# Kernel tuning notes

Measured on AMD Instinct MI355X. Metric: run time of the kernel, lower is better.

Reference implementation:

```python
import jax, jax.numpy as jnp
import numpy as np

ITERATIONS = 3
EPS = 1e-06

def squash(s):
    # square_norm along last dim, keepdims (matches torch squash)
    sq = jnp.sum(s * s, axis=-1, keepdims=True)
    return sq / (1.0 + sq) * s / (jnp.sqrt(sq) + EPS)

def setup_inputs() -> dict:
    key = jax.random.key(0)
    k1, k2 = jax.random.split(key)
    x = jax.random.normal(k1, (64, 32, 8, 8, 16), dtype=jnp.float32)
    W = jax.random.normal(k2, (1, 32, 8, 8, 32, 16, 32), dtype=jnp.float32)
    return {"x": x, "W": W}

def reference(x, W):
    # u_hat: (B, C, H, Wd, O, D) = x (B,C,H,Wd,I) @ W (C,H,Wd,O,I,D)
    u_hat = jnp.einsum('bchwi,chwoid->bchwod', x, W[0])
    b = jnp.zeros(u_hat.shape[:-1], dtype=u_hat.dtype)  # (B,C,H,Wd,O)
    for _ in range(ITERATIONS - 1):
        c = jax.nn.softmax(b, axis=-1)
        s = jnp.sum(c[..., None] * u_hat, axis=(1, 2, 3))  # (B,O,D)
        v = squash(s)
        b = b + jnp.sum(u_hat * v[:, None, None, None], axis=-1)
    c = jax.nn.softmax(b, axis=-1)
    s = jnp.sum(c[..., None] * u_hat, axis=(1, 2, 3))
    return squash(s)  # (B, out_capsules, out_cap_dim)
```

## Files before the change

### kernel.cpp

```cpp
#include <hip/hip_runtime.h>
#include <math.h>

#define B_ 64
#define N_ 2048
#define O_ 32
#define I_ 16
#define D_ 32
#define OD_ 1024

typedef __attribute__((ext_vector_type(8))) short bf16x8;
typedef __attribute__((ext_vector_type(4))) float f32x4;

union FragU { unsigned u[4]; uint4 v; bf16x8 f; };

__device__ __forceinline__ void barrier_lds() {
  asm volatile("s_waitcnt lgkmcnt(0)\n\ts_barrier" ::: "memory");
}

template <int CTRL>
__device__ __forceinline__ float dpp_mov_f(float x) {
  return __int_as_float(
      __builtin_amdgcn_update_dpp(0, __float_as_int(x), CTRL, 0xf, 0xf, true));
}
__device__ __forceinline__ float row16_sum(float x) {
  x += dpp_mov_f<0x128>(x);
  x += dpp_mov_f<0x124>(x);
  x += dpp_mov_f<0x4e>(x);
  x += dpp_mov_f<0xb1>(x);
  return x;
}
__device__ __forceinline__ float grp32_max(float x) {
  x = fmaxf(x, dpp_mov_f<0xb1>(x));
  x = fmaxf(x, dpp_mov_f<0x4e>(x));
  x = fmaxf(x, dpp_mov_f<0x124>(x));
  x = fmaxf(x, dpp_mov_f<0x128>(x));
  x = fmaxf(x, __shfl_xor(x, 16));
  return x;
}
__device__ __forceinline__ float grp32_sum(float x) {
  x += dpp_mov_f<0xb1>(x);
  x += dpp_mov_f<0x4e>(x);
  x += dpp_mov_f<0x124>(x);
  x += dpp_mov_f<0x128>(x);
  x += __shfl_xor(x, 16);
  return x;
}

__device__ __forceinline__ void dk_split(float f, unsigned &h, unsigned &l) {
  unsigned u = __float_as_uint(f);
  h = u & 0xffff0000u;
  float lo = f - __uint_as_float(h);
  l = __float_as_uint(lo) >> 16;
}
__device__ __forceinline__ void dk_split16(float f, unsigned short &h,
                                           unsigned short &l) {
  unsigned u = __float_as_uint(f);
  unsigned hu = u & 0xffff0000u;
  h = (unsigned short)(u >> 16);
  float lo = f - __uint_as_float(hu);
  l = (unsigned short)(__float_as_uint(lo) >> 16);
}
__device__ __forceinline__ unsigned pk(unsigned short e0, unsigned short e1) {
  return (unsigned)e0 | ((unsigned)e1 << 16);
}

__global__ __launch_bounds__(256) void prep_all(const float* __restrict__ W,
                                                const float* __restrict__ x,
                                                uint4* __restrict__ WP,
                                                uint4* __restrict__ XP) {
  if (blockIdx.x < 8192) {
    int t = blockIdx.x * 256 + threadIdx.x;
    int d = t & 31, o = (t >> 5) & 31, n = t >> 10;
    const float* wp = W + ((size_t)(n * O_ + o) * I_) * D_ + d;
    unsigned short hh[I_], ll[I_];
#pragma unroll
    for (int i = 0; i < I_; ++i) dk_split16(wp[i * D_], hh[i], ll[i]);
    int c = d & 15, dhalf = d >> 4;
    size_t base = ((size_t)(n * O_ + o) * 2 + dhalf) * 4;
#pragma unroll
    for (int sel = 0; sel < 2; ++sel) {
      const unsigned short* e = sel ? ll : hh;
#pragma unroll
      for (int qp = 0; qp < 2; ++qp) {
        uint4 u;
        u.x = pk(e[qp * 8 + 0], e[qp * 8 + 1]);
        u.y = pk(e[qp * 8 + 2], e[qp * 8 + 3]);
        u.z = pk(e[qp * 8 + 4], e[qp * 8 + 5]);
        u.w = pk(e[qp * 8 + 6], e[qp * 8 + 7]);
        WP[(base + sel * 2 + qp) * 16 + c] = u;
      }
    }
  } else {
    int t = (blockIdx.x - 8192) * 256 + threadIdx.x;
    int c = t & 15, n = (t >> 4) & 2047, bg = t >> 15;
    const float* xp = x + ((size_t)(bg * 16 + c) * N_ + n) * I_;
    unsigned short hh[I_], ll[I_];
#pragma unroll
    for (int i = 0; i < I_; ++i) dk_split16(xp[i], hh[i], ll[i]);
    size_t base = ((size_t)bg * N_ + n) * 4;
#pragma unroll
    for (int sel = 0; sel < 2; ++sel) {
      const unsigned short* e = sel ? ll : hh;
#pragma unroll
      for (int qp = 0; qp < 2; ++qp) {
        uint4 u;
        u.x = pk(e[qp * 8 + 0], e[qp * 8 + 1]);
        u.y = pk(e[qp * 8 + 2], e[qp * 8 + 3]);
        u.z = pk(e[qp * 8 + 4], e[qp * 8 + 5]);
        u.w = pk(e[qp * 8 + 6], e[qp * 8 + 7]);
        XP[(base + sel * 2 + qp) * 16 + c] = u;
      }
    }
  }
}

template <int UNIFORM>
__global__ __launch_bounds__(1024, 4) void mfma_pass6(
    const uint4* __restrict__ XP, const uint4* __restrict__ WP,
    const float* __restrict__ v, float* __restrict__ partial, int NC) {
  const int tid = threadIdx.x;
  const int lane = tid & 63;
  const int w = tid >> 6;
  const int q = lane >> 4;
  const int c = lane & 15;
  const int qp = q & 1;
  const int ch = blockIdx.x;
  const int bgy = blockIdx.y;

  __shared__ uint4 xps[2][16][4][16];
  __shared__ float ls_logit[32 * O_];
  __shared__ float ls_c[32 * O_];

  const int n0 = ch * NC;

  {
    uint4* xf = (uint4*)xps;
    const int total = 2 * NC * 64;
    for (int l = tid; l < total; l += 1024) {
      int bgl = l / (NC * 64);
      int rest = l - bgl * (NC * 64);
      xf[bgl * 1024 + rest] =
          XP[(size_t)(bgy * 2 + bgl) * 131072 + (size_t)n0 * 64 + rest];
    }
  }

  f32x4 s_t[2][4];
#pragma unroll
  for (int bgl = 0; bgl < 2; ++bgl)
#pragma unroll
    for (int ct = 0; ct < 4; ++ct) s_t[bgl][ct] = (f32x4){0.f, 0.f, 0.f, 0.f};

  float vreg[2][4][4];
  if (!UNIFORM) {
#pragma unroll
    for (int bgl = 0; bgl < 2; ++bgl)
#pragma unroll
      for (int ct = 0; ct < 4; ++ct) {
        int odc = (2 * w + (ct >> 1)) * 32 + (ct & 1) * 16 + c;
#pragma unroll
        for (int r = 0; r < 4; ++r)
          vreg[bgl][ct][r] =
              v[(size_t)(bgy * 32 + bgl * 16 + q * 4 + r) * OD_ + odc];
      }
  }

  barrier_lds();

  const uint4* wbase = WP + (size_t)(2 * w) * 128 + lane;

  for (int nl = 0; nl < NC; ++nl) {
    const size_t n = (size_t)(n0 + nl);

    FragU cb[4];
#pragma unroll
    for (int ct = 0; ct < 4; ++ct) cb[ct].v = wbase[n * 4096 + ct * 64];

    if (UNIFORM) {
#pragma unroll
      for (int bgl = 0; bgl < 2; ++bgl) {
        FragU ah, al;
        ah.v = xps[bgl][nl][qp][c];
        al.v = xps[bgl][nl][2 + qp][c];
#pragma unroll
        for (int ct = 0; ct < 4; ++ct) {
          s_t[bgl][ct] = __builtin_amdgcn_mfma_f32_16x16x32_bf16(
              ah.f, cb[ct].f, s_t[bgl][ct], 0, 0, 0);
          s_t[bgl][ct] = __builtin_amdgcn_mfma_f32_16x16x32_bf16(
              al.f, cb[ct].f, s_t[bgl][ct], 0, 0, 0);
        }
      }
    } else {
      float lg[2][2][4];
#pragma unroll
      for (int bgl = 0; bgl < 2; ++bgl)
#pragma unroll
        for (int ol = 0; ol < 2; ++ol)
#pragma unroll
          for (int r = 0; r < 4; ++r) lg[bgl][ol][r] = 0.f;
#pragma unroll
      for (int bgl = 0; bgl < 2; ++bgl) {
        FragU ah, al;
        ah.v = xps[bgl][nl][qp][c];
        al.v = xps[bgl][nl][2 + qp][c];
#pragma unroll
        for (int ct = 0; ct < 4; ++ct) {
          f32x4 acc = (f32x4){0.f, 0.f, 0.f, 0.f};
          acc = __builtin_amdgcn_mfma_f32_16x16x32_bf16(ah.f, cb[ct].f, acc, 0, 0, 0);
          f32x4 u = __builtin_amdgcn_mfma_f32_16x16x32_bf16(al.f, cb[ct].f, acc, 0, 0, 0);
          int ol = ct >> 1;
#pragma unroll
          for (int r = 0; r < 4; ++r)
            lg[bgl][ol][r] = fmaf(u[r], vreg[bgl][ct][r], lg[bgl][ol][r]);
        }
      }
#pragma unroll
      for (int bgl = 0; bgl < 2; ++bgl)
#pragma unroll
        for (int ol = 0; ol < 2; ++ol)
#pragma unroll
          for (int r = 0; r < 4; ++r) lg[bgl][ol][r] = row16_sum(lg[bgl][ol][r]);
      if (c == 0) {
#pragma unroll
        for (int bgl = 0; bgl < 2; ++bgl)
#pragma unroll
          for (int ol = 0; ol < 2; ++ol)
#pragma unroll
            for (int r = 0; r < 4; ++r)
              ls_logit[(bgl * 16 + q * 4 + r) * O_ + 2 * w + ol] = lg[bgl][ol][r];
      }
      barrier_lds();
      {
        float l = ls_logit[tid];
        float mx = grp32_max(l);
        float e = __expf(l - mx);
        float sm = grp32_sum(e);
        ls_c[tid] = e / sm;
      }
      barrier_lds();
#pragma unroll
      for (int bgl = 0; bgl < 2; ++bgl) {
        FragU ah, al;
        ah.v = xps[bgl][nl][qp][c];
        al.v = xps[bgl][nl][2 + qp][c];
#pragma unroll
        for (int ct = 0; ct < 4; ++ct) {
          f32x4 acc = (f32x4){0.f, 0.f, 0.f, 0.f};
          acc = __builtin_amdgcn_mfma_f32_16x16x32_bf16(ah.f, cb[ct].f, acc, 0, 0, 0);
          f32x4 u = __builtin_amdgcn_mfma_f32_16x16x32_bf16(al.f, cb[ct].f, acc, 0, 0, 0);
          int o = 2 * w + (ct >> 1);
#pragma unroll
          for (int r = 0; r < 4; ++r) {
            float cc = ls_c[(bgl * 16 + q * 4 + r) * O_ + o];
            s_t[bgl][ct][r] = fmaf(cc, u[r], s_t[bgl][ct][r]);
          }
        }
      }
    }
  }

  const float scale = UNIFORM ? (1.f / 32.f) : 1.f;
#pragma unroll
  for (int bgl = 0; bgl < 2; ++bgl)
#pragma unroll
    for (int ct = 0; ct < 4; ++ct) {
      int odc = (2 * w + (ct >> 1)) * 32 + (ct & 1) * 16 + c;
#pragma unroll
      for (int r = 0; r < 4; ++r) {
        partial[((size_t)ch * B_ + bgy * 32 + bgl * 16 + q * 4 + r) * OD_ + odc] =
            s_t[bgl][ct][r] * scale;
      }
    }
}

template <int UNIFORM>
__global__ __launch_bounds__(512, 4) void mfma_pass_fb(
    const float* __restrict__ x, const float* __restrict__ W,
    const float* __restrict__ v, float* __restrict__ partial, int NC) {
  const int tid = threadIdx.x;
  const int lane = tid & 63;
  const int cg = tid >> 6;
  const int q = lane >> 4;
  const int c = lane & 15;
  const int ch = blockIdx.x;
  const int bg = blockIdx.y;

  __shared__ float ls_logit[16 * O_];
  __shared__ float ls_c[16 * O_];

  f32x4 s_t[8];
#pragma unroll
  for (int ct = 0; ct < 8; ++ct) s_t[ct] = (f32x4){0.f, 0.f, 0.f, 0.f};

  const int n0 = ch * NC;
  const int ih = (q & 1) * 8;
  const float* xrow = x + ((size_t)(bg * 16 + c) * N_) * I_ + ih;

  for (int nl = 0; nl < NC; ++nl) {
    const int n = n0 + nl;
    const float* xp = xrow + (size_t)n * I_;
    float4 xv0 = *(const float4*)xp;
    float4 xv1 = *(const float4*)(xp + 4);
    float xv[8] = {xv0.x, xv0.y, xv0.z, xv0.w, xv1.x, xv1.y, xv1.z, xv1.w};
    FragU a1;
#pragma unroll
    for (int p = 0; p < 4; ++p) {
      unsigned h0, l0, h1, l1;
      dk_split(xv[2 * p], h0, l0);
      dk_split(xv[2 * p + 1], h1, l1);
      a1.u[p] = (q < 2) ? ((h0 >> 16) | h1) : (l0 | (l1 << 16));
    }
    f32x4 u_t[8];
#pragma unroll
    for (int ct = 0; ct < 8; ++ct) {
      const int o = cg * 4 + (ct >> 1);
      const int d = (ct & 1) * 16 + c;
      const float* wp = W + (((size_t)n * O_ + o) * I_ + ih) * D_ + d;
      FragU b1, b2;
#pragma unroll
      for (int p = 0; p < 4; ++p) {
        unsigned h0, l0, h1, l1;
        dk_split(wp[(2 * p) * D_], h0, l0);
        dk_split(wp[(2 * p + 1) * D_], h1, l1);
        b1.u[p] = (h0 >> 16) | h1;
        b2.u[p] = l0 | (l1 << 16);
      }
      if (UNIFORM) {
        s_t[ct] = __builtin_amdgcn_mfma_f32_16x16x32_bf16(a1.f, b1.f, s_t[ct], 0, 0, 0);
        s_t[ct] = __builtin_amdgcn_mfma_f32_16x16x32_bf16(a1.f, b2.f, s_t[ct], 0, 0, 0);
      } else {
        f32x4 acc = (f32x4){0.f, 0.f, 0.f, 0.f};
        acc = __builtin_amdgcn_mfma_f32_16x16x32_bf16(a1.f, b1.f, acc, 0, 0, 0);
        u_t[ct] = __builtin_amdgcn_mfma_f32_16x16x32_bf16(a1.f, b2.f, acc, 0, 0, 0);
      }
    }
    if (!UNIFORM) {
#pragma unroll
      for (int ol = 0; ol < 4; ++ol) {
        float lg[4] = {0.f, 0.f, 0.f, 0.f};
#pragma unroll
        for (int hf = 0; hf < 2; ++hf) {
          int ct = ol * 2 + hf;
          int odc = cg * 128 + ct * 16 + c;
#pragma unroll
          for (int r = 0; r < 4; ++r)
            lg[r] = fmaf(u_t[ct][r], v[(size_t)(bg * 16 + q * 4 + r) * OD_ + odc], lg[r]);
        }
#pragma unroll
        for (int r = 0; r < 4; ++r) {
#pragma unroll
          for (int m = 1; m < 16; m <<= 1) lg[r] += __shfl_xor(lg[r], m);
        }
        if (c == 0) {
#pragma unroll
          for (int r = 0; r < 4; ++r)
            ls_logit[(q * 4 + r) * O_ + cg * 4 + ol] = lg[r];
        }
      }
      __syncthreads();
      {
        int b_l = tid >> 5, o = tid & 31;
        float l = ls_logit[b_l * O_ + o];
        float mx = l;
#pragma unroll
        for (int m = 16; m >= 1; m >>= 1) mx = fmaxf(mx, __shfl_xor(mx, m));
        float e = __expf(l - mx);
        float sm = e;
#pragma unroll
        for (int m = 16; m >= 1; m >>= 1) sm += __shfl_xor(sm, m);
        ls_c[b_l * O_ + o] = e / sm;
      }
      __syncthreads();
#pragma unroll
      for (int ol = 0; ol < 4; ++ol) {
        int o = cg * 4 + ol;
        float cc[4];
#pragma unroll
        for (int r = 0; r < 4; ++r) cc[r] = ls_c[(q * 4 + r) * O_ + o];
#pragma unroll
        for (int hf = 0; hf < 2; ++hf) {
          int ct = ol * 2 + hf;
#pragma unroll
          for (int r = 0; r < 4; ++r)
            s_t[ct][r] = fmaf(cc[r], u_t[ct][r], s_t[ct][r]);
        }
      }
    }
  }

  const float scale = UNIFORM ? (1.f / 32.f) : 1.f;
#pragma unroll
  for (int ct = 0; ct < 8; ++ct) {
#pragma unroll
    for (int r = 0; r < 4; ++r) {
      partial[((size_t)ch * B_ + bg * 16 + q * 4 + r) * OD_ + cg * 128 + ct * 16 + c] =
          s_t[ct][r] * scale;
    }
  }
}

__global__ __launch_bounds__(256) void reduce_stageA(float4* __restrict__ part,
                                                     int cq) {
  int qa = blockIdx.x >> 6;
  int g4 = (blockIdx.x & 63) * 256 + threadIdx.x;
  float4 s = make_float4(0.f, 0.f, 0.f, 0.f);
  for (int i = 0; i < cq; ++i) {
    float4 p = part[(size_t)(qa * cq + i) * 16384 + g4];
    s.x += p.x; s.y += p.y; s.z += p.z; s.w += p.w;
  }
  part[(size_t)(qa * cq) * 16384 + g4] = s;
}

__global__ __launch_bounds__(256) void reduce_stageB(
    const float4* __restrict__ part, int cq, const float4* __restrict__ prev,
    float4* __restrict__ out) {
  int g4 = blockIdx.x * 256 + threadIdx.x;
  float4 s = make_float4(0.f, 0.f, 0.f, 0.f);
#pragma unroll
  for (int qa = 0; qa < 4; ++qa) {
    float4 p = part[(size_t)(qa * cq) * 16384 + g4];
    s.x += p.x; s.y += p.y; s.z += p.z; s.w += p.w;
  }
  float sq = s.x * s.x + s.y * s.y + s.z * s.z + s.w * s.w;
#pragma unroll
  for (int m = 4; m >= 1; m >>= 1) sq += __shfl_xor(sq, m, 8);
  float scale = sq / ((1.f + sq) * (sqrtf(sq) + 1e-6f));
  float4 r = make_float4(s.x * scale, s.y * scale, s.z * scale, s.w * scale);
  if (prev) {
    float4 p = prev[g4];
    r.x += p.x; r.y += p.y; r.z += p.z; r.w += p.w;
  }
  out[g4] = r;
}

__global__ __launch_bounds__(256) void reduce_squash(
    const float4* __restrict__ part, int chunks,
    const float4* __restrict__ prev, float4* __restrict__ out) {
  int g4 = blockIdx.x * 256 + threadIdx.x;
  float4 s = make_float4(0.f, 0.f, 0.f, 0.f);
#pragma unroll 4
  for (int ch = 0; ch < chunks; ++ch) {
    float4 p = part[(size_t)ch * 16384 + g4];
    s.x += p.x; s.y += p.y; s.z += p.z; s.w += p.w;
  }
  float sq = s.x * s.x + s.y * s.y + s.z * s.z + s.w * s.w;
#pragma unroll
  for (int m = 4; m >= 1; m >>= 1) sq += __shfl_xor(sq, m, 8);
  float scale = sq / ((1.f + sq) * (sqrtf(sq) + 1e-6f));
  float4 r = make_float4(s.x * scale, s.y * scale, s.z * scale, s.w * scale);
  if (prev) {
    float4 p = prev[g4];
    r.x += p.x; r.y += p.y; r.z += p.z; r.w += p.w;
  }
  out[g4] = r;
}

extern "C" void kernel_launch(void* const* d_in, const int* in_sizes, int n_in,
                              void* d_out, int out_size, void* d_ws,
                              size_t ws_size, hipStream_t stream) {
  const float* x = (const float*)d_in[0];
  const float* W = (const float*)d_in[1];
  float* out = (float*)d_out;

  const size_t XP_FLOATS = 4ull * 2048 * 4 * 16 * 4;
  const size_t WP_FLOATS = 2048ull * 32 * 2 * 4 * 16 * 4;

  float* v1 = (float*)d_ws;
  float* vsum = v1 + 65536;
  float* partial = vsum + 65536;

  const int chunks = 128;
  bool packed_path =
      (131072 + (size_t)chunks * 65536 + XP_FLOATS + WP_FLOATS) * 4 <= ws_size;

  if (packed_path) {
    uint4* XP = (uint4*)(partial + (size_t)chunks * 65536);
    uint4* WP = XP + XP_FLOATS / 4;
    const int NC = N_ / chunks;
    const int cq = chunks / 4;
    dim3 grid(chunks, 2);

    prep_all<<<8704, 256, 0, stream>>>(W, x, WP, XP);

    mfma_pass6<1><<<grid, 1024, 0, stream>>>(XP, WP, nullptr, partial, NC);
    reduce_stageA<<<256, 256, 0, stream>>>((float4*)partial, cq);
    reduce_stageB<<<64, 256, 0, stream>>>((const float4*)partial, cq, nullptr,
                                          (float4*)v1);
    mfma_pass6<0><<<grid, 1024, 0, stream>>>(XP, WP, v1, partial, NC);
    reduce_stageA<<<256, 256, 0, stream>>>((float4*)partial, cq);
    reduce_stageB<<<64, 256, 0, stream>>>((const float4*)partial, cq,
                                          (const float4*)v1, (float4*)vsum);
    mfma_pass6<0><<<grid, 1024, 0, stream>>>(XP, WP, vsum, partial, NC);
    reduce_stageA<<<256, 256, 0, stream>>>((float4*)partial, cq);
    reduce_stageB<<<64, 256, 0, stream>>>((const float4*)partial, cq, nullptr,
                                          (float4*)out);
  } else {
    int fchunks = 128;
    while (fchunks > 1 && (131072 + (size_t)fchunks * 65536) * 4 > ws_size)
      fchunks >>= 1;
    int NC = N_ / fchunks;
    dim3 grid(fchunks, 4);

    mfma_pass_fb<1><<<grid, 512, 0, stream>>>(x, W, nullptr, partial, NC);
    reduce_squash<<<64, 256, 0, stream>>>((const float4*)partial, fchunks,
                                          nullptr, (float4*)v1);
    mfma_pass_fb<0><<<grid, 512, 0, stream>>>(x, W, v1, partial, NC);
    reduce_squash<<<64, 256, 0, stream>>>((const float4*)partial, fchunks,
                                          (const float4*)v1, (float4*)vsum);
    mfma_pass_fb<0><<<grid, 512, 0, stream>>>(x, W, vsum, partial, NC);
    reduce_squash<<<64, 256, 0, stream>>>((const float4*)partial, fchunks,
                                          nullptr, (float4*)out);
  }
}
```

Baseline: 413.0 us.

## Fuse W bf16 split packing into first uniform routing pass

```diff
diff --git a/kernel.cpp b/kernel.cpp
--- a/kernel.cpp
+++ b/kernel.cpp
@@ -64,54 +64,133 @@
   return (unsigned)e0 | ((unsigned)e1 << 16);
 }
 
-__global__ __launch_bounds__(256) void prep_all(const float* __restrict__ W,
-                                                const float* __restrict__ x,
-                                                uint4* __restrict__ WP,
-                                                uint4* __restrict__ XP) {
-  if (blockIdx.x < 8192) {
-    int t = blockIdx.x * 256 + threadIdx.x;
-    int d = t & 31, o = (t >> 5) & 31, n = t >> 10;
-    const float* wp = W + ((size_t)(n * O_ + o) * I_) * D_ + d;
-    unsigned short hh[I_], ll[I_];
-#pragma unroll
-    for (int i = 0; i < I_; ++i) dk_split16(wp[i * D_], hh[i], ll[i]);
-    int c = d & 15, dhalf = d >> 4;
-    size_t base = ((size_t)(n * O_ + o) * 2 + dhalf) * 4;
-#pragma unroll
-    for (int sel = 0; sel < 2; ++sel) {
-      const unsigned short* e = sel ? ll : hh;
-#pragma unroll
-      for (int qp = 0; qp < 2; ++qp) {
-        uint4 u;
-        u.x = pk(e[qp * 8 + 0], e[qp * 8 + 1]);
-        u.y = pk(e[qp * 8 + 2], e[qp * 8 + 3]);
-        u.z = pk(e[qp * 8 + 4], e[qp * 8 + 5]);
-        u.w = pk(e[qp * 8 + 6], e[qp * 8 + 7]);
-        WP[(base + sel * 2 + qp) * 16 + c] = u;
-      }
-    }
-  } else {
-    int t = (blockIdx.x - 8192) * 256 + threadIdx.x;
-    int c = t & 15, n = (t >> 4) & 2047, bg = t >> 15;
-    const float* xp = x + ((size_t)(bg * 16 + c) * N_ + n) * I_;
-    unsigned short hh[I_], ll[I_];
-#pragma unroll
-    for (int i = 0; i < I_; ++i) dk_split16(xp[i], hh[i], ll[i]);
-    size_t base = ((size_t)bg * N_ + n) * 4;
-#pragma unroll
-    for (int sel = 0; sel < 2; ++sel) {
-      const unsigned short* e = sel ? ll : hh;
-#pragma unroll
-      for (int qp = 0; qp < 2; ++qp) {
-        uint4 u;
-        u.x = pk(e[qp * 8 + 0], e[qp * 8 + 1]);
-        u.y = pk(e[qp * 8 + 2], e[qp * 8 + 3]);
-        u.z = pk(e[qp * 8 + 4], e[qp * 8 + 5]);
-        u.w = pk(e[qp * 8 + 6], e[qp * 8 + 7]);
-        XP[(base + sel * 2 + qp) * 16 + c] = u;
-      }
-    }
-  }
+__global__ __launch_bounds__(256) void prep_x(const float* __restrict__ x,
+                                              uint4* __restrict__ XP) {
+  int t = blockIdx.x * 256 + threadIdx.x;
+  int c = t & 15, n = (t >> 4) & 2047, bg = t >> 15;
+  const float* xp = x + ((size_t)(bg * 16 + c) * N_ + n) * I_;
+  unsigned short hh[I_], ll[I_];
+#pragma unroll
+  for (int i = 0; i < I_; ++i) dk_split16(xp[i], hh[i], ll[i]);
+  size_t base = ((size_t)bg * N_ + n) * 4;
+#pragma unroll
+  for (int sel = 0; sel < 2; ++sel) {
+    const unsigned short* e = sel ? ll : hh;
+#pragma unroll
+    for (int qp = 0; qp < 2; ++qp) {
+      uint4 u;
+      u.x = pk(e[qp * 8 + 0], e[qp * 8 + 1]);
+      u.y = pk(e[qp * 8 + 2], e[qp * 8 + 3]);
+      u.z = pk(e[qp * 8 + 4], e[qp * 8 + 5]);
+      u.w = pk(e[qp * 8 + 6], e[qp * 8 + 7]);
+      XP[(base + sel * 2 + qp) * 16 + c] = u;
+    }
+  }
+}
+
+__global__ __launch_bounds__(256) void prep_w(const float* __restrict__ W,
+                                              uint4* __restrict__ WP) {
+  int t = blockIdx.x * 256 + threadIdx.x;
+  int d = t & 31, o = (t >> 5) & 31, n = t >> 10;
+  const float* wp = W + ((size_t)(n * O_ + o) * I_) * D_ + d;
+  unsigned short hh[I_], ll[I_];
+#pragma unroll
+  for (int i = 0; i < I_; ++i) dk_split16(wp[i * D_], hh[i], ll[i]);
+  int c = d & 15, dhalf = d >> 4;
+  size_t base = ((size_t)(n * O_ + o) * 2 + dhalf) * 4;
+#pragma unroll
+  for (int sel = 0; sel < 2; ++sel) {
+    const unsigned short* e = sel ? ll : hh;
+#pragma unroll
+    for (int qp = 0; qp < 2; ++qp) {
+      uint4 u;
+      u.x = pk(e[qp * 8 + 0], e[qp * 8 + 1]);
+      u.y = pk(e[qp * 8 + 2], e[qp * 8 + 3]);
+      u.z = pk(e[qp * 8 + 4], e[qp * 8 + 5]);
+      u.w = pk(e[qp * 8 + 6], e[qp * 8 + 7]);
+      WP[(base + sel * 2 + qp) * 16 + c] = u;
+    }
+  }
+}
+
+__global__ __launch_bounds__(1024, 4) void fused_w1(
+    const float* __restrict__ W, const uint4* __restrict__ XP,
+    uint4* __restrict__ WP, float* __restrict__ partial, int NC) {
+  const int tid = threadIdx.x;
+  const int lane = tid & 63;
+  const int w = tid >> 6;
+  const int q = lane >> 4;
+  const int c = lane & 15;
+  const int qp = q & 1;
+  const int ch = blockIdx.x;
+  const int n0 = ch * NC;
+
+  __shared__ uint4 xps2[4][8][4][16];
+
+  {
+    uint4* xf = (uint4*)xps2;
+    const int total = 4 * 8 * 64;
+    for (int l = tid; l < total; l += 1024) {
+      int bg = l >> 9;
+      int rest = l & 511;
+      xf[l] = XP[(size_t)bg * 131072 + (size_t)n0 * 64 + rest];
+    }
+  }
+
+  f32x4 s_t[4][4];
+#pragma unroll
+  for (int bg = 0; bg < 4; ++bg)
+#pragma unroll
+    for (int ct = 0; ct < 4; ++ct) s_t[bg][ct] = (f32x4){0.f, 0.f, 0.f, 0.f};
+
+  __syncthreads();
+
+  for (int nl = 0; nl < NC; ++nl) {
+    const size_t n = (size_t)(n0 + nl);
+#pragma unroll
+    for (int ct = 0; ct < 4; ++ct) {
+      const int ol = ct >> 1, dh = ct & 1;
+      const int o = 2 * w + ol;
+      const float* wpp = W + (((size_t)n * O_ + o) * I_ + qp * 8) * D_ + dh * 16 + c;
+      float w8[8];
+#pragma unroll
+      for (int j = 0; j < 8; ++j) w8[j] = wpp[j * D_];
+      FragU b1, b2;
+#pragma unroll
+      for (int p = 0; p < 4; ++p) {
+        unsigned short h0, l0, h1, l1;
+        dk_split16(w8[2 * p], h0, l0);
+        dk_split16(w8[2 * p + 1], h1, l1);
+        b1.u[p] = pk(h0, h1);
+        b2.u[p] = pk(l0, l1);
+      }
+      FragU cb;
+      cb.v = (q < 2) ? b1.v : b2.v;
+      WP[n * 4096 + o * 128 + dh * 64 + lane] = cb.v;
+#pragma unroll
+      for (int bg = 0; bg < 4; ++bg) {
+        FragU ah, al;
+        ah.v = xps2[bg][nl][qp][c];
+        al.v = xps2[bg][nl][2 + qp][c];
+        s_t[bg][ct] = __builtin_amdgcn_mfma_f32_16x16x32_bf16(
+            ah.f, cb.f, s_t[bg][ct], 0, 0, 0);
+        s_t[bg][ct] = __builtin_amdgcn_mfma_f32_16x16x32_bf16(
+            al.f, cb.f, s_t[bg][ct], 0, 0, 0);
+      }
+    }
+  }
+
+#pragma unroll
+  for (int bg = 0; bg < 4; ++bg)
+#pragma unroll
+    for (int ct = 0; ct < 4; ++ct) {
+      int odc = (2 * w + (ct >> 1)) * 32 + (ct & 1) * 16 + c;
+#pragma unroll
+      for (int r = 0; r < 4; ++r) {
+        partial[((size_t)ch * B_ + bg * 16 + q * 4 + r) * OD_ + odc] =
+            s_t[bg][ct][r] * (1.f / 32.f);
+      }
+    }
 }
 
 template <int UNIFORM>
@@ -468,30 +547,48 @@
   float* vsum = v1 + 65536;
   float* partial = vsum + 65536;
 
-  const int chunks = 128;
-  bool packed_path =
-      (131072 + (size_t)chunks * 65536 + XP_FLOATS + WP_FLOATS) * 4 <= ws_size;
-
-  if (packed_path) {
-    uint4* XP = (uint4*)(partial + (size_t)chunks * 65536);
+  const size_t need256 =
+      (131072 + 256ull * 65536 + XP_FLOATS + WP_FLOATS) * 4;
+  const size_t need128 =
+      (131072 + 128ull * 65536 + XP_FLOATS + WP_FLOATS) * 4;
+
+  if (ws_size >= need256) {
+    uint4* XP = (uint4*)(partial + 256ull * 65536);
     uint4* WP = XP + XP_FLOATS / 4;
-    const int NC = N_ / chunks;
-    const int cq = chunks / 4;
-    dim3 grid(chunks, 2);
-
-    prep_all<<<8704, 256, 0, stream>>>(W, x, WP, XP);
-
-    mfma_pass6<1><<<grid, 1024, 0, stream>>>(XP, WP, nullptr, partial, NC);
-    reduce_stageA<<<256, 256, 0, stream>>>((float4*)partial, cq);
-    reduce_stageB<<<64, 256, 0, stream>>>((const float4*)partial, cq, nullptr,
+
+    prep_x<<<512, 256, 0, stream>>>(x, XP);
+    fused_w1<<<256, 1024, 0, stream>>>(W, XP, WP, partial, 8);
+    reduce_stageA<<<256, 256, 0, stream>>>((float4*)partial, 64);
+    reduce_stageB<<<64, 256, 0, stream>>>((const float4*)partial, 64, nullptr,
                                           (float4*)v1);
-    mfma_pass6<0><<<grid, 1024, 0, stream>>>(XP, WP, v1, partial, NC);
-    reduce_stageA<<<256, 256, 0, stream>>>((float4*)partial, cq);
-    reduce_stageB<<<64, 256, 0, stream>>>((const float4*)partial, cq,
+    dim3 grid(128, 2);
+    mfma_pass6<0><<<grid, 1024, 0, stream>>>(XP, WP, v1, partial, 16);
+    reduce_stageA<<<256, 256, 0, stream>>>((float4*)partial, 32);
+    reduce_stageB<<<64, 256, 0, stream>>>((const float4*)partial, 32,
                                           (const float4*)v1, (float4*)vsum);
-    mfma_pass6<0><<<grid, 1024, 0, stream>>>(XP, WP, vsum, partial, NC);
-    reduce_stageA<<<256, 256, 0, stream>>>((float4*)partial, cq);
-    reduce_stageB<<<64, 256, 0, stream>>>((const float4*)partial, cq, nullptr,
+    mfma_pass6<0><<<grid, 1024, 0, stream>>>(XP, WP, vsum, partial, 16);
+    reduce_stageA<<<256, 256, 0, stream>>>((float4*)partial, 32);
+    reduce_stageB<<<64, 256, 0, stream>>>((const float4*)partial, 32, nullptr,
+                                          (float4*)out);
+  } else if (ws_size >= need128) {
+    uint4* XP = (uint4*)(partial + 128ull * 65536);
+    uint4* WP = XP + XP_FLOATS / 4;
+    dim3 grid(128, 2);
+
+    prep_x<<<512, 256, 0, stream>>>(x, XP);
+    prep_w<<<8192, 256, 0, stream>>>(W, WP);
+
+    mfma_pass6<1><<<grid, 1024, 0, stream>>>(XP, WP, nullptr, partial, 16);
+    reduce_stageA<<<256, 256, 0, stream>>>((float4*)partial, 32);
+    reduce_stageB<<<64, 256, 0, stream>>>((const float4*)partial, 32, nullptr,
+                                          (float4*)v1);
+    mfma_pass6<0><<<grid, 1024, 0, stream>>>(XP, WP, v1, partial, 16);
+    reduce_stageA<<<256, 256, 0, stream>>>((float4*)partial, 32);
+    reduce_stageB<<<64, 256, 0, stream>>>((const float4*)partial, 32,
+                                          (const float4*)v1, (float4*)vsum);
+    mfma_pass6<0><<<grid, 1024, 0, stream>>>(XP, WP, vsum, partial, 16);
+    reduce_stageA<<<256, 256, 0, stream>>>((float4*)partial, 32);
+    reduce_stageB<<<64, 256, 0, stream>>>((const float4*)partial, 32, nullptr,
                                           (float4*)out);
   } else {
     int fchunks = 128;
```

New measurement: 446.3 us. 1.08x slower.
